# Kernel tuning notes

Hardware: AMD Instinct MI355X
Metric: run time of the kernel (lower is better)

## Reference

```python
import math
import jax, jax.numpy as jnp
import numpy as np

EMBD_DIM = 1024
N_HEADS = 16
WINDOW = 9           # odd, per assert
STRIDE = WINDOW // 2 # 4
BS, T = 4, 4096      # t % stride == 0


def setup_inputs() -> dict:
    key = jax.random.key(0)
    ks = jax.random.split(key, 8)
    c = EMBD_DIM
    std = 0.02
    inp = {
        "q": jax.random.normal(ks[0], (BS, c, T), dtype=jnp.float32),
        "q_mask": jnp.ones((BS, 1, T), dtype=bool),
        # 1x1 Conv1d projections == pointwise linear: W (out, in), b (out,)
        "Wq": jax.random.normal(ks[1], (c, c), dtype=jnp.float32) * std,
        "bq": jnp.zeros((c,), dtype=jnp.float32),
        "Wk": jax.random.normal(ks[2], (c, c), dtype=jnp.float32) * std,
        "bk": jnp.zeros((c,), dtype=jnp.float32),
        "Wv": jax.random.normal(ks[3], (c, c), dtype=jnp.float32) * std,
        "bv": jnp.zeros((c,), dtype=jnp.float32),
        "Wp": jax.random.normal(ks[4], (c, c), dtype=jnp.float32) * std,
        "bp": jnp.zeros((c,), dtype=jnp.float32),
    }
    return inp


def _pointwise(x, W, b):
    # 1x1 Conv1d on (bs, c, t)
    return jnp.einsum('oc,bct->bot', W, x) + b[None, :, None]


def reference(q, q_mask, Wq, bq, Wk, bk, Wv, bv, Wp, bp):
    bs, c, t = q.shape
    h, w, s = N_HEADS, WINDOW, STRIDE
    d = c // h
    scale = 1.0 / math.sqrt(d)

    qq = _pointwise(q, Wq, bq)
    kk = _pointwise(q, Wk, bk)  # self-attention: k = v = q
    vv = _pointwise(q, Wv, bv)

    def split_heads(x):  # (bs, c, t) -> (bs*h, t, d)
        return x.reshape(bs, h, d, t).transpose(0, 1, 3, 2).reshape(bs * h, t, d)

    qh = split_heads(qq) * scale
    kh = split_heads(kk)
    vh = split_heads(vv)

    # Sliding-window indices: query i attends to keys j in [i-s, i+s].
    # This is exactly the band produced by the chunked as_strided code plus
    # its l_mask/r_mask boundary fills (which mask j < 0 and j >= t).
    offs = jnp.arange(-s, s + 1)                 # (w,)
    idx = jnp.arange(t)[:, None] + offs[None, :] # (t, w)
    in_range = (idx >= 0) & (idx < t)
    idxc = jnp.clip(idx, 0, t - 1)

    k_win = kh[:, idxc]                          # (bs*h, t, w, d)
    scores = jnp.einsum('ntd,ntwd->ntw', qh, k_win)
    scores = scores.reshape(bs, h, t, w)

    # kv mask: invalid key positions contribute -10000 (as in _attn_normalize)
    kv_valid = q_mask.reshape(bs, t)
    kv_bias = jnp.where(kv_valid[:, idxc], 0.0, -10000.0)  # (bs, t, w)
    scores = scores + kv_bias[:, None]
    scores = jnp.where(in_range[None, None], scores, -jnp.inf)

    attn = jax.nn.softmax(scores, axis=-1)
    # zero attention rows at invalid query positions
    attn = jnp.where(kv_valid[:, None, :, None], attn, 0.0)
    attn = attn.reshape(bs * h, t, w)

    v_win = vh[:, idxc]                          # (bs*h, t, w, d)
    out = jnp.einsum('ntw,ntwd->ntd', attn, v_win)

    out = out.reshape(bs, h, t, d).transpose(0, 1, 3, 2).reshape(bs, c, t)
    out = _pointwise(out, Wp, bp) * q_mask.astype(out.dtype)
    return (out, q_mask)
```

## Files before the change

### kernel.cpp

```cpp
#include <hip/hip_runtime.h>
#include <hip/hip_bf16.h>
#include <math.h>

#define T_SEQ 4096
#define C_DIM 1024
#define NH    16
#define HD    64
#define BSZ   4
#define VSTRIDE 4120
#define VPAD    12

typedef __attribute__((ext_vector_type(8))) short bf16x8;
typedef __attribute__((ext_vector_type(4))) float f32x4;

__device__ __forceinline__ unsigned short f2bf(float f) {
    union { __hip_bfloat16 h; unsigned short u; } cv;
    cv.h = __float2bfloat16(f);
    return cv.u;
}

__global__ __launch_bounds__(256) void conv_w_kernel(
    const float* __restrict__ Wq, const float* __restrict__ Wk,
    const float* __restrict__ Wv, const float* __restrict__ Wp,
    __hip_bfloat16* __restrict__ Wqkv, __hip_bfloat16* __restrict__ Wpb)
{
    int i = blockIdx.x * 256 + threadIdx.x;
    int which = i >> 18;
    int off = (i & 262143) << 2;
    const float* src = which == 0 ? Wq : which == 1 ? Wk : which == 2 ? Wv : Wp;
    float4 v = *reinterpret_cast<const float4*>(src + off);
    ushort4 o;
    o.x = f2bf(v.x); o.y = f2bf(v.y); o.z = f2bf(v.z); o.w = f2bf(v.w);
    __hip_bfloat16* dst = (which < 3) ? (Wqkv + ((size_t)which << 20) + off) : (Wpb + off);
    *reinterpret_cast<ushort4*>(dst) = o;
}

__global__ __launch_bounds__(256) void transpose_x_kernel(
    const float* __restrict__ q, __hip_bfloat16* __restrict__ xT)
{
    __shared__ float tile[64][65];
    int t0 = blockIdx.x * 64;
    int c0 = blockIdx.y * 64;
    int b  = blockIdx.z;
    int tx = threadIdx.x & 63;
    int ty = threadIdx.x >> 6;
    const float* src = q + ((size_t)b * C_DIM + c0) * T_SEQ + t0;
    #pragma unroll
    for (int i = 0; i < 16; ++i) {
        int c = ty + i * 4;
        tile[c][tx] = src[(size_t)c * T_SEQ + tx];
    }
    __syncthreads();
    __hip_bfloat16* dst = xT + ((size_t)b * T_SEQ + t0) * C_DIM + c0;
    #pragma unroll
    for (int i = 0; i < 16; ++i) {
        int t = ty + i * 4;
        dst[(size_t)t * C_DIM + tx] = __float2bfloat16(tile[tx][t]);
    }
}

__device__ __forceinline__ void stage_half(
    const __hip_bfloat16* __restrict__ Abase, const __hip_bfloat16* __restrict__ Bbase,
    __hip_bfloat16* Alds, __hip_bfloat16* Blds, int slot, int kbase, int tid, int wid)
{
    __hip_bfloat16* As = Alds + slot * 8192;
    __hip_bfloat16* Bs = Blds + slot * 8192;
    #pragma unroll
    for (int i = 0; i < 2; ++i) {
        int q = i * 512 + tid;
        int r = q >> 2;
        int s4 = (q & 3) ^ ((r >> 1) & 3);
        const __hip_bfloat16* sa = Abase + (size_t)r * C_DIM + kbase + s4 * 8;
        __builtin_amdgcn_global_load_lds(
            (const __attribute__((address_space(1))) void*)sa,
            (__attribute__((address_space(3))) void*)(As + (i * 512 + wid * 64) * 8), 16, 0, 0);
        const __hip_bfloat16* sb = Bbase + (size_t)r * C_DIM + kbase + s4 * 8;
        __builtin_amdgcn_global_load_lds(
            (const __attribute__((address_space(1))) void*)sb,
            (__attribute__((address_space(3))) void*)(Bs + (i * 512 + wid * 64) * 8), 16, 0, 0);
    }
}

#define GEMM_PIPELINE_CORE()                                                          \
    f32x4 acc[8][4] = {};                                                             \
    stage_half(Abase, Bbase, Alds, Blds, 0, 0, tid, wid);                             \
    stage_half(Abase, Bbase, Alds, Blds, 1, 32, tid, wid);                            \
    const int NKT = C_DIM / 64;                                                       \
    for (int kt = 0; kt < NKT; ++kt) {                                                \
        _Pragma("unroll")                                                             \
        for (int ks = 0; ks < 2; ++ks) {                                              \
            if (kt == NKT - 1 && ks == 1)                                             \
                asm volatile("s_waitcnt vmcnt(0)" ::: "memory");                      \
            else                                                                      \
                asm volatile("s_waitcnt vmcnt(4)" ::: "memory");                      \
            __builtin_amdgcn_s_barrier();                                             \
            asm volatile("" ::: "memory");                                            \
            int s = ((kt & 1) << 1) | ks;                                             \
            if (kt + 1 < NKT)                                                         \
                stage_half(Abase, Bbase, Alds, Blds, s ^ 2,                           \
                           (kt + 1) * 64 + ks * 32, tid, wid);                        \
            const __hip_bfloat16* As = Alds + s * 8192;                               \
            const __hip_bfloat16* Bs = Blds + s * 8192;                               \
            bf16x8 af[8], bfr[4];                                                     \
            _Pragma("unroll")                                                         \
            for (int mi = 0; mi < 8; ++mi)                                            \
                af[mi] = *reinterpret_cast<const bf16x8*>(                            \
                    As + (wr * 128 + mi * 16 + fr) * 32 + sof);                       \
            _Pragma("unroll")                                                         \
            for (int ni = 0; ni < 4; ++ni)                                            \
                bfr[ni] = *reinterpret_cast<const bf16x8*>(                           \
                    Bs + (wc * 64 + ni * 16 + fr) * 32 + sof);                        \
            __builtin_amdgcn_s_setprio(1);                                            \
            _Pragma("unroll")                                                         \
            for (int mi = 0; mi < 8; ++mi) {                                          \
                _Pragma("unroll")                                                     \
                for (int ni = 0; ni < 4; ++ni)                                        \
                    acc[mi][ni] = __builtin_amdgcn_mfma_f32_16x16x32_bf16(            \
                        af[mi], bfr[ni], acc[mi][ni], 0, 0, 0);                       \
            }                                                                         \
            __builtin_amdgcn_s_setprio(0);                                            \
        }                                                                             \
    }

__global__ __launch_bounds__(512, 2) void gemm_qkv_kernel(
    const __hip_bfloat16* __restrict__ A,
    const __hip_bfloat16* __restrict__ xT,
    const float* __restrict__ bq, const float* __restrict__ bk, const float* __restrict__ bv,
    __hip_bfloat16* __restrict__ qh, __hip_bfloat16* __restrict__ kh,
    __hip_bfloat16* __restrict__ vhT)
{
    __shared__ __align__(16) __hip_bfloat16 Alds[4 * 8192];
    __shared__ __align__(16) __hip_bfloat16 Blds[4 * 8192];
    int tid  = threadIdx.x;
    int lane = tid & 63;
    int wid  = tid >> 6;
    int wr = wid >> 2;
    int wc = wid & 3;
    int fr = lane & 15;
    int g  = lane >> 4;
    int sof = (g ^ ((fr >> 1) & 3)) * 8;
    int n0 = blockIdx.x * 256;
    int m0 = blockIdx.y * 256;
    int b  = blockIdx.z;
    const __hip_bfloat16* Abase = A + (size_t)m0 * C_DIM;
    const __hip_bfloat16* Bbase = xT + ((size_t)b * T_SEQ + n0) * C_DIM;

    GEMM_PIPELINE_CORE()

    #pragma unroll
    for (int mi = 0; mi < 8; ++mi) {
        int mrow = m0 + wr * 128 + mi * 16 + g * 4;
        int which = mrow >> 10;
        int o = mrow & 1023;
        int hh = o >> 6, dd = o & 63;
        const float* bias = which == 0 ? bq : which == 1 ? bk : bv;
        float b0 = bias[o], b1 = bias[o + 1], b2 = bias[o + 2], b3 = bias[o + 3];
        if (which == 2) {
            size_t rowd = ((size_t)b * NH + hh) * HD + dd;
            #pragma unroll
            for (int ni = 0; ni < 4; ++ni) {
                int t = n0 + wc * 64 + ni * 16 + fr;
                vhT[(rowd + 0) * VSTRIDE + VPAD + t] = __float2bfloat16(acc[mi][ni][0] + b0);
                vhT[(rowd + 1) * VSTRIDE + VPAD + t] = __float2bfloat16(acc[mi][ni][1] + b1);
                vhT[(rowd + 2) * VSTRIDE + VPAD + t] = __float2bfloat16(acc[mi][ni][2] + b2);
                vhT[(rowd + 3) * VSTRIDE + VPAD + t] = __float2bfloat16(acc[mi][ni][3] + b3);
            }
        } else {
            __hip_bfloat16* outp = which == 0 ? qh : kh;
            size_t hb = ((size_t)b * NH + hh) * T_SEQ;
            #pragma unroll
            for (int ni = 0; ni < 4; ++ni) {
                int t = n0 + wc * 64 + ni * 16 + fr;
                ushort4 pk;
                pk.x = f2bf(acc[mi][ni][0] + b0);
                pk.y = f2bf(acc[mi][ni][1] + b1);
                pk.z = f2bf(acc[mi][ni][2] + b2);
                pk.w = f2bf(acc[mi][ni][3] + b3);
                *reinterpret_cast<ushort4*>(outp + (hb + t) * HD + dd) = pk;
            }
        }
    }
}

__global__ __launch_bounds__(512, 2) void gemm_proj_kernel(
    const __hip_bfloat16* __restrict__ A,
    const __hip_bfloat16* __restrict__ xT,
    const float* __restrict__ bp,
    const int* __restrict__ mask,
    float* __restrict__ out)
{
    __shared__ __align__(16) __hip_bfloat16 Alds[4 * 8192];
    __shared__ __align__(16) __hip_bfloat16 Blds[4 * 8192];
    int tid  = threadIdx.x;
    int lane = tid & 63;
    int wid  = tid >> 6;
    int wr = wid >> 2;
    int wc = wid & 3;
    int fr = lane & 15;
    int g  = lane >> 4;
    int sof = (g ^ ((fr >> 1) & 3)) * 8;
    int n0 = blockIdx.x * 256;
    int m0 = blockIdx.y * 256;
    int b  = blockIdx.z;
    const __hip_bfloat16* Abase = A + (size_t)m0 * C_DIM;
    const __hip_bfloat16* Bbase = xT + ((size_t)b * T_SEQ + n0) * C_DIM;

    GEMM_PIPELINE_CORE()

    #pragma unroll
    for (int mi = 0; mi < 8; ++mi) {
        int orow = m0 + wr * 128 + mi * 16 + g * 4;
        float b0 = bp[orow], b1 = bp[orow + 1], b2 = bp[orow + 2], b3 = bp[orow + 3];
        #pragma unroll
        for (int ni = 0; ni < 4; ++ni) {
            int t = n0 + wc * 64 + ni * 16 + fr;
            float mval = (mask[b * T_SEQ + t] != 0) ? 1.0f : 0.0f;
            size_t obase = ((size_t)b * C_DIM + orow) * T_SEQ + t;
            out[obase]             = (acc[mi][ni][0] + b0) * mval;
            out[obase + T_SEQ]     = (acc[mi][ni][1] + b1) * mval;
            out[obase + 2 * T_SEQ] = (acc[mi][ni][2] + b2) * mval;
            out[obase + 3 * T_SEQ] = (acc[mi][ni][3] + b3) * mval;
        }
    }
}

__global__ __launch_bounds__(256) void attn_kernel(
    const __hip_bfloat16* __restrict__ qh,
    const __hip_bfloat16* __restrict__ kh,
    const __hip_bfloat16* __restrict__ vhT,
    const int* __restrict__ mask,
    __hip_bfloat16* __restrict__ attnT)
{
    __shared__ __hip_bfloat16 Plds[4][16 * 40];
    int lane = threadIdx.x & 63;
    int wid  = threadIdx.x >> 6;
    int gw = blockIdx.x * 4 + wid;
    int bh = gw >> 7;
    int tg = gw & 127;
    int b = bh >> 4, h = bh & 15;
    size_t kqbase = (size_t)bh * T_SEQ * HD;
    const int* mrow = mask + b * T_SEQ;
    int fr = lane & 15;
    int g  = lane >> 4;
    char* pby = (char*)(&Plds[wid][0]);
    f32x4 zacc = {};

    for (int it = 0; it < 2; ++it) {
        int t0 = tg * 32 + it * 16;
        bf16x8 qB[2], kA[2][2];
        #pragma unroll
        for (int ks = 0; ks < 2; ++ks)
            qB[ks] = *reinterpret_cast<const bf16x8*>(qh + kqbase + (size_t)(t0 + fr) * HD + ks * 32 + g * 8);
        #pragma unroll
        for (int mt = 0; mt < 2; ++mt) {
            int kr = t0 - 4 + mt * 16 + fr;
            kr = min(max(kr, 0), T_SEQ - 1);
            #pragma unroll
            for (int ks = 0; ks < 2; ++ks)
                kA[mt][ks] = *reinterpret_cast<const bf16x8*>(kh + kqbase + (size_t)kr * HD + ks * 32 + g * 8);
        }
        f32x4 sacc[2] = {zacc, zacc};
        #pragma unroll
        for (int mt = 0; mt < 2; ++mt)
            #pragma unroll
            for (int ks = 0; ks < 2; ++ks)
                sacc[mt] = __builtin_amdgcn_mfma_f32_16x16x32_bf16(kA[mt][ks], qB[ks], sacc[mt], 0, 0, 0);

        float ev[2][4];
        float mx = -INFINITY;
        #pragma unroll
        for (int mt = 0; mt < 2; ++mt) {
            #pragma unroll
            for (int r = 0; r < 4; ++r) {
                int j = mt * 16 + g * 4 + r;
                int jg = t0 - 4 + j;
                int w = j - fr;
                int jc = min(max(jg, 0), T_SEQ - 1);
                float sv = sacc[mt][r] * 0.125f + (mrow[jc] != 0 ? 0.0f : -10000.0f);
                bool valid = (w >= 0) && (w <= 8) && (jg >= 0) && (jg < T_SEQ);
                ev[mt][r] = valid ? sv : -INFINITY;
                mx = fmaxf(mx, ev[mt][r]);
            }
        }
        mx = fmaxf(mx, __shfl_xor(mx, 16));
        mx = fmaxf(mx, __shfl_xor(mx, 32));
        float ss = 0.0f;
        #pragma unroll
        for (int mt = 0; mt < 2; ++mt) {
            #pragma unroll
            for (int r = 0; r < 4; ++r) {
                float e2 = __expf(ev[mt][r] - mx);
                ev[mt][r] = e2;
                ss += e2;
            }
        }
        ss += __shfl_xor(ss, 16);
        ss += __shfl_xor(ss, 32);
        float inv = 1.0f / ss;

        #pragma unroll
        for (int mt = 0; mt < 2; ++mt) {
            unsigned int lo = (unsigned int)f2bf(ev[mt][0] * inv) | ((unsigned int)f2bf(ev[mt][1] * inv) << 16);
            unsigned int hi = (unsigned int)f2bf(ev[mt][2] * inv) | ((unsigned int)f2bf(ev[mt][3] * inv) << 16);
            int jb = (mt * 16 + g * 4) * 2;
            *reinterpret_cast<unsigned int*>(pby + fr * 80 + jb)     = lo;
            *reinterpret_cast<unsigned int*>(pby + fr * 80 + jb + 4) = hi;
        }
        bf16x8 pB = *reinterpret_cast<const bf16x8*>(pby + fr * 80 + g * 16);

        int t = t0 + fr;
        float mq = (mrow[t] != 0) ? 1.0f : 0.0f;
        #pragma unroll
        for (int dt = 0; dt < 4; ++dt) {
            bf16x8 vA = *reinterpret_cast<const bf16x8*>(
                vhT + ((size_t)bh * HD + dt * 16 + fr) * VSTRIDE + VPAD + (t0 - 4) + g * 8);
            f32x4 o = __builtin_amdgcn_mfma_f32_16x16x32_bf16(vA, pB, zacc, 0, 0, 0);
            ushort4 pk;
            pk.x = f2bf(o[0] * mq);
            pk.y = f2bf(o[1] * mq);
            pk.z = f2bf(o[2] * mq);
            pk.w = f2bf(o[3] * mq);
            *reinterpret_cast<ushort4*>(attnT + ((size_t)b * T_SEQ + t) * C_DIM + h * HD + dt * 16 + g * 4) = pk;
        }
    }
}

__global__ __launch_bounds__(256) void mask_echo_kernel(
    const int* __restrict__ mask, float* __restrict__ out)
{
    int i = blockIdx.x * 256 + threadIdx.x;
    if (i < BSZ * T_SEQ) out[i] = (mask[i] != 0) ? 1.0f : 0.0f;
}

extern "C" void kernel_launch(void* const* d_in, const int* in_sizes, int n_in,
                              void* d_out, int out_size, void* d_ws, size_t ws_size,
                              hipStream_t stream)
{
    const float* q     = (const float*)d_in[0];
    const int*   qmask = (const int*)d_in[1];
    const float* Wq    = (const float*)d_in[2];
    const float* bq    = (const float*)d_in[3];
    const float* Wk    = (const float*)d_in[4];
    const float* bk    = (const float*)d_in[5];
    const float* Wv    = (const float*)d_in[6];
    const float* bv    = (const float*)d_in[7];
    const float* Wp    = (const float*)d_in[8];
    const float* bp    = (const float*)d_in[9];
    float* out = (float*)d_out;

    char* ws = (char*)d_ws;
    __hip_bfloat16* Wqkv  = (__hip_bfloat16*)(ws);
    __hip_bfloat16* Wpb   = (__hip_bfloat16*)(ws + 6291456);
    __hip_bfloat16* xT    = (__hip_bfloat16*)(ws + 8388608);
    __hip_bfloat16* attnT = (__hip_bfloat16*)(ws + 8388608);
    __hip_bfloat16* qh    = (__hip_bfloat16*)(ws + 41943040);
    __hip_bfloat16* kh    = (__hip_bfloat16*)(ws + 75497472);
    __hip_bfloat16* vhT   = (__hip_bfloat16*)(ws + 109051904);

    conv_w_kernel<<<4096, 256, 0, stream>>>(Wq, Wk, Wv, Wp, Wqkv, Wpb);
    transpose_x_kernel<<<dim3(64, 16, 4), 256, 0, stream>>>(q, xT);
    gemm_qkv_kernel<<<dim3(16, 12, 4), 512, 0, stream>>>(Wqkv, xT, bq, bk, bv, qh, kh, vhT);
    attn_kernel<<<2048, 256, 0, stream>>>(qh, kh, vhT, qmask, attnT);
    gemm_proj_kernel<<<dim3(16, 4, 4), 512, 0, stream>>>(Wpb, attnT, bp, qmask, out);
    mask_echo_kernel<<<64, 256, 0, stream>>>(qmask, out + (size_t)BSZ * C_DIM * T_SEQ);
}
```

Before: 242.0 us.

## Restructure GEMM main loop into ping-pong half-tile phases with split staging

Replaces the two-substep k-loop with a flat loop over 32-wide k slices, each split into two phases that handle half of the M fragments. The async A and B tile loads are issued in separate phases, and extra barriers plus lgkmcnt waits are placed so that waves interleave LDS reads, global-to-LDS staging and MFMA bursts. The aim is better overlap of memory traffic with matrix-core work and less register pressure from fragments. The cost is more barriers per slice, and the vmcnt accounting is hand-tuned, so it is fragile.

```diff
diff --git a/kernel.cpp b/kernel.cpp
--- a/kernel.cpp
+++ b/kernel.cpp
@@ -59,67 +59,75 @@
     }
 }
 
-__device__ __forceinline__ void stage_half(
-    const __hip_bfloat16* __restrict__ Abase, const __hip_bfloat16* __restrict__ Bbase,
-    __hip_bfloat16* Alds, __hip_bfloat16* Blds, int slot, int kbase, int tid, int wid)
-{
-    __hip_bfloat16* As = Alds + slot * 8192;
-    __hip_bfloat16* Bs = Blds + slot * 8192;
+__device__ __forceinline__ void stage_mat(
+    const __hip_bfloat16* __restrict__ base,
+    __hip_bfloat16* lds_slot, int kbase, int tid, int wid)
+{
     #pragma unroll
     for (int i = 0; i < 2; ++i) {
-        int q = i * 512 + tid;
-        int r = q >> 2;
-        int s4 = (q & 3) ^ ((r >> 1) & 3);
-        const __hip_bfloat16* sa = Abase + (size_t)r * C_DIM + kbase + s4 * 8;
+        int c = i * 512 + tid;
+        int r = c >> 2;
+        int sg = (c & 3) ^ ((r >> 1) & 3);
+        const __hip_bfloat16* src = base + (size_t)r * C_DIM + kbase + sg * 8;
         __builtin_amdgcn_global_load_lds(
-            (const __attribute__((address_space(1))) void*)sa,
-            (__attribute__((address_space(3))) void*)(As + (i * 512 + wid * 64) * 8), 16, 0, 0);
-        const __hip_bfloat16* sb = Bbase + (size_t)r * C_DIM + kbase + s4 * 8;
-        __builtin_amdgcn_global_load_lds(
-            (const __attribute__((address_space(1))) void*)sb,
-            (__attribute__((address_space(3))) void*)(Bs + (i * 512 + wid * 64) * 8), 16, 0, 0);
-    }
-}
-
-#define GEMM_PIPELINE_CORE()                                                          \
-    f32x4 acc[8][4] = {};                                                             \
-    stage_half(Abase, Bbase, Alds, Blds, 0, 0, tid, wid);                             \
-    stage_half(Abase, Bbase, Alds, Blds, 1, 32, tid, wid);                            \
-    const int NKT = C_DIM / 64;                                                       \
-    for (int kt = 0; kt < NKT; ++kt) {                                                \
-        _Pragma("unroll")                                                             \
-        for (int ks = 0; ks < 2; ++ks) {                                              \
-            if (kt == NKT - 1 && ks == 1)                                             \
-                asm volatile("s_waitcnt vmcnt(0)" ::: "memory");                      \
-            else                                                                      \
-                asm volatile("s_waitcnt vmcnt(4)" ::: "memory");                      \
-            __builtin_amdgcn_s_barrier();                                             \
-            asm volatile("" ::: "memory");                                            \
-            int s = ((kt & 1) << 1) | ks;                                             \
-            if (kt + 1 < NKT)                                                         \
-                stage_half(Abase, Bbase, Alds, Blds, s ^ 2,                           \
-                           (kt + 1) * 64 + ks * 32, tid, wid);                        \
-            const __hip_bfloat16* As = Alds + s * 8192;                               \
-            const __hip_bfloat16* Bs = Blds + s * 8192;                               \
-            bf16x8 af[8], bfr[4];                                                     \
-            _Pragma("unroll")                                                         \
-            for (int mi = 0; mi < 8; ++mi)                                            \
-                af[mi] = *reinterpret_cast<const bf16x8*>(                            \
-                    As + (wr * 128 + mi * 16 + fr) * 32 + sof);                       \
-            _Pragma("unroll")                                                         \
-            for (int ni = 0; ni < 4; ++ni)                                            \
-                bfr[ni] = *reinterpret_cast<const bf16x8*>(                           \
-                    Bs + (wc * 64 + ni * 16 + fr) * 32 + sof);                        \
-            __builtin_amdgcn_s_setprio(1);                                            \
-            _Pragma("unroll")                                                         \
-            for (int mi = 0; mi < 8; ++mi) {                                          \
-                _Pragma("unroll")                                                     \
-                for (int ni = 0; ni < 4; ++ni)                                        \
-                    acc[mi][ni] = __builtin_amdgcn_mfma_f32_16x16x32_bf16(            \
-                        af[mi], bfr[ni], acc[mi][ni], 0, 0, 0);                       \
-            }                                                                         \
-            __builtin_amdgcn_s_setprio(0);                                            \
-        }                                                                             \
+            (const __attribute__((address_space(1))) void*)src,
+            (__attribute__((address_space(3))) void*)(lds_slot + (i * 512 + wid * 64) * 8),
+            16, 0, 0);
+    }
+}
+
+#define GEMM_PIPELINE_CORE()                                                         \
+    f32x4 acc[8][4] = {};                                                            \
+    stage_mat(Abase, Alds + 0 * 8192, 0, tid, wid);                                  \
+    stage_mat(Bbase, Blds + 0 * 8192, 0, tid, wid);                                  \
+    stage_mat(Abase, Alds + 1 * 8192, 32, tid, wid);                                 \
+    stage_mat(Bbase, Blds + 1 * 8192, 32, tid, wid);                                 \
+    asm volatile("s_waitcnt vmcnt(4)" ::: "memory");                                 \
+    __builtin_amdgcn_s_barrier();                                                    \
+    const int NST = C_DIM / 32;                                                      \
+    for (int st = 0; st < NST; ++st) {                                               \
+        const __hip_bfloat16* As = Alds + (st & 3) * 8192;                           \
+        const __hip_bfloat16* Bs = Blds + (st & 3) * 8192;                           \
+        bf16x8 bfr[4];                                                               \
+        _Pragma("unroll")                                                            \
+        for (int mih = 0; mih < 2; ++mih) {                                          \
+            if (st + 2 < NST) {                                                      \
+                if (mih == 0)                                                        \
+                    stage_mat(Abase, Alds + ((st + 2) & 3) * 8192, (st + 2) * 32, tid, wid); \
+                else                                                                 \
+                    stage_mat(Bbase, Blds + ((st + 2) & 3) * 8192, (st + 2) * 32, tid, wid); \
+            }                                                                        \
+            if (mih == 0) {                                                          \
+                _Pragma("unroll")                                                    \
+                for (int ni = 0; ni < 4; ++ni)                                       \
+                    bfr[ni] = *reinterpret_cast<const bf16x8*>(                      \
+                        Bs + (wc * 64 + ni * 16 + fr) * 32 + sof);                   \
+            }                                                                        \
+            bf16x8 af[4];                                                            \
+            _Pragma("unroll")                                                        \
+            for (int q2 = 0; q2 < 4; ++q2)                                           \
+                af[q2] = *reinterpret_cast<const bf16x8*>(                           \
+                    As + (wr * 128 + (mih * 4 + q2) * 16 + fr) * 32 + sof);          \
+            __builtin_amdgcn_s_barrier();                                            \
+            asm volatile("s_waitcnt lgkmcnt(0)" ::: "memory");                       \
+            __builtin_amdgcn_sched_barrier(0);                                       \
+            __builtin_amdgcn_s_setprio(1);                                           \
+            _Pragma("unroll")                                                        \
+            for (int q2 = 0; q2 < 4; ++q2) {                                         \
+                _Pragma("unroll")                                                    \
+                for (int ni = 0; ni < 4; ++ni)                                       \
+                    acc[mih * 4 + q2][ni] = __builtin_amdgcn_mfma_f32_16x16x32_bf16( \
+                        af[q2], bfr[ni], acc[mih * 4 + q2][ni], 0, 0, 0);            \
+            }                                                                        \
+            __builtin_amdgcn_s_setprio(0);                                           \
+            if (mih == 1) {                                                          \
+                if (st == NST - 2)                                                   \
+                    asm volatile("s_waitcnt vmcnt(0)" ::: "memory");                 \
+                else if (st < NST - 2)                                               \
+                    asm volatile("s_waitcnt vmcnt(4)" ::: "memory");                 \
+            }                                                                        \
+            __builtin_amdgcn_s_barrier();                                            \
+        }                                                                            \
     }
 
 __global__ __launch_bounds__(512, 2) void gemm_qkv_kernel(
```

New measurement: 277.6 us. 14.7% more time.
